# Optimization experiments

Hardware: AMD Instinct MI355X
Metric: run time of the kernel (lower is better)

Reference implementation:

```python
import jax, jax.numpy as jnp
import numpy as np

BATCH, SEQ, IN_DIM, HID, STATE, NLAYERS, OUT = 32, 2048, 32, 512, 64, 4, 2
EPS = 1e-5


def layer_norm(x, g, b):
    m = jnp.mean(x, axis=-1, keepdims=True)
    v = jnp.mean((x - m) ** 2, axis=-1, keepdims=True)
    return (x - m) / jnp.sqrt(v + EPS) * g + b


def s4_layer(x, A, C, D, g, b):
    # x: (B, L, H); A, C: (H, S); D: (H,)
    xn = layer_norm(x, g, b)
    u = jnp.swapaxes(xn, 0, 1)  # (L, B, H)

    def step(h, u_t):
        h = jnp.tanh(u_t @ A + h)          # (B, S)
        y = h @ C.T + u_t * D              # (B, H)
        return h, y

    h0 = jnp.zeros((x.shape[0], A.shape[1]), dtype=x.dtype)
    _, ys = jax.lax.scan(step, h0, u)
    return jnp.swapaxes(ys, 0, 1) + x      # residual


def setup_inputs() -> dict:
    key = jax.random.key(0)
    ks = jax.random.split(key, 16)
    s_in = 1.0 / np.sqrt(IN_DIM)
    s_h = 1.0 / np.sqrt(HID)
    s_h2 = 1.0 / np.sqrt(HID // 2)
    return {
        "x": jax.random.normal(ks[0], (BATCH, SEQ, IN_DIM), jnp.float32),
        "Win": jax.random.uniform(ks[1], (IN_DIM, HID), jnp.float32, -s_in, s_in),
        "bin_": jax.random.uniform(ks[2], (HID,), jnp.float32, -s_in, s_in),
        "A": jax.random.normal(ks[3], (NLAYERS, HID, STATE), jnp.float32) * 0.05,
        "C": jax.random.normal(ks[4], (NLAYERS, HID, STATE), jnp.float32) * 0.05,
        "Dvec": jax.random.normal(ks[5], (NLAYERS, HID), jnp.float32),
        "ln_g": jnp.ones((NLAYERS, HID), jnp.float32),
        "ln_b": jnp.zeros((NLAYERS, HID), jnp.float32),
        "norm_g": jnp.ones((HID,), jnp.float32),
        "norm_b": jnp.zeros((HID,), jnp.float32),
        "W1": jax.random.uniform(ks[6], (HID, HID // 2), jnp.float32, -s_h, s_h),
        "b1": jax.random.uniform(ks[7], (HID // 2,), jnp.float32, -s_h, s_h),
        "W2": jax.random.uniform(ks[8], (HID // 2, OUT), jnp.float32, -s_h2, s_h2),
        "b2": jax.random.uniform(ks[9], (OUT,), jnp.float32, -s_h2, s_h2),
    }


def reference(x, Win, bin_, A, C, Dvec, ln_g, ln_b, norm_g, norm_b, W1, b1, W2, b2):
    h = x @ Win + bin_                      # (B, L, H)
    for i in range(A.shape[0]):
        h = s4_layer(h, A[i], C[i], Dvec[i], ln_g[i], ln_b[i])
    h = layer_norm(h, norm_g, norm_b)
    h = h[:, -1, :]                         # last timestep
    h = jax.nn.gelu(h @ W1 + b1, approximate=False)  # torch nn.GELU uses erf
    return h @ W2 + b2
```

## Files before the change

### kernel.cpp

```cpp
#include <hip/hip_runtime.h>

#define BATCH   32
#define SEQ     2048
#define IN_DIM  32
#define HID     512
#define STATE   64
#define NLAYERS 4
#define NTOK    (BATCH*SEQ)
#define EPS     1e-5f
#define KTAN    2.8853900817779268f
#define NCHUNK  32
#define WARMUP  32

#define CF4(p) (*reinterpret_cast<const float4*>(p))

typedef __attribute__((ext_vector_type(8))) short short8v;
typedef __attribute__((ext_vector_type(4))) float f32x4;

__device__ __forceinline__ float fast_exp2(float x){ return __builtin_amdgcn_exp2f(x); }
__device__ __forceinline__ float fast_rcp(float x){ return __builtin_amdgcn_rcpf(x); }
__device__ __forceinline__ short f2bf(float f){
  unsigned u = __float_as_uint(f);
  unsigned r = (u + 0x7FFF + ((u>>16)&1)) >> 16;
  return (short)r;
}
__device__ __forceinline__ float bf2f(short s){
  return __uint_as_float(((unsigned)(unsigned short)s) << 16);
}

__global__ __launch_bounds__(256) void k_prep(
    const float* __restrict__ A, const float* __restrict__ g,
    const float* __restrict__ b, const float* __restrict__ Win,
    const float* __restrict__ bin, const float* __restrict__ C,
    short* __restrict__ ApT, float* __restrict__ GA, float* __restrict__ BA,
    short* __restrict__ WA1Th, short* __restrict__ WA1Tl,
    float* __restrict__ binA, short* __restrict__ Cb, short* __restrict__ WinT)
{
  __shared__ float red[4][64], red2[4][64];
  int tid = threadIdx.x;
  int s = tid & 63, part = tid >> 6;
  int blk = blockIdx.x;
  if (blk < NLAYERS){
    int l = blk;
    const float* Al = A + l*HID*STATE;
    const float* Cl = C + l*HID*STATE;
    const float* gl = g + l*HID;
    const float* bl = b + l*HID;
    float ga=0.f, ba=0.f;
    for (int j=part*128; j<(part+1)*128; ++j){
      float a  = Al[j*STATE+s];
      float ap = gl[j]*a;
      ApT[l*HID*STATE + s*HID + j] = f2bf(ap);
      Cb[l*HID*STATE + j*STATE + s] = f2bf(Cl[j*STATE+s]);
      ga += ap; ba = fmaf(bl[j], a, ba);
    }
    red[part][s]=ga; red2[part][s]=ba;
    __syncthreads();
    if (tid < 64){
      GA[l*STATE+s] = red[0][s]+red[1][s]+red[2][s]+red[3][s];
      BA[l*STATE+s] = red2[0][s]+red2[1][s]+red2[2][s]+red2[3][s];
    }
  } else if (blk < NLAYERS+32){
    int k = blk - NLAYERS;
    const float* w = Win + k*HID;
    float acc = 0.f;
    for (int j=part*128; j<(part+1)*128; ++j)
      acc = fmaf(w[j], g[j]*A[j*STATE+s], acc);
    red[part][s] = acc;
    __syncthreads();
    if (tid < 64){
      float v = red[0][s]+red[1][s]+red[2][s]+red[3][s];
      short hi = f2bf(v);
      WA1Th[s*IN_DIM + k] = hi;
      WA1Tl[s*IN_DIM + k] = f2bf(v - bf2f(hi));
    }
  } else if (blk == NLAYERS+32){
    float acc = 0.f;
    for (int j=part*128; j<(part+1)*128; ++j)
      acc = fmaf(bin[j], g[j]*A[j*STATE+s], acc);
    red[part][s] = acc;
    __syncthreads();
    if (tid < 64) binA[s] = red[0][s]+red[1][s]+red[2][s]+red[3][s];
  } else {
    for (int e = tid; e < HID*IN_DIM; e += 256){
      int cc = e >> 5, k = e & 31;
      WinT[cc*IN_DIM + k] = f2bf(Win[k*HID + cc]);
    }
  }
}

__global__ __launch_bounds__(256) void k_input(const float* __restrict__ x,
    const short* __restrict__ WinT, const float* __restrict__ bin,
    const short* __restrict__ WA1Th, const short* __restrict__ WA1Tl,
    const float* __restrict__ binA,
    const float* __restrict__ GA0, const float* __restrict__ BA0,
    short* __restrict__ h, float* __restrict__ U, float2* __restrict__ stats)
{
  __shared__ __align__(16) short xhi[64][72];
  __shared__ __align__(16) short xlo[64][72];
  int m0 = blockIdx.x * 64;
  int tid = threadIdx.x;
  int w = tid >> 6, lane = tid & 63;
  int c = lane & 15, q = lane >> 4;
  #pragma unroll
  for (int i=0;i<8;i++){
    int idx = tid + i*256;
    int row = idx >> 5, k = idx & 31;
    float v = x[(size_t)(m0+row)*IN_DIM + k];
    short hi = f2bf(v);
    xhi[row][k] = hi;
    xlo[row][k] = f2bf(v - bf2f(hi));
  }
  __syncthreads();
  short8v ah = *reinterpret_cast<const short8v*>(&xhi[w*16 + c][q*8]);
  short8v al = *reinterpret_cast<const short8v*>(&xlo[w*16 + c][q*8]);
  float sum[4]={0.f,0.f,0.f,0.f}, sq[4]={0.f,0.f,0.f,0.f};
  for (int jc=0; jc<HID; jc+=64){
    f32x4 acc[4];
    #pragma unroll
    for (int t=0;t<4;t++){
      short8v bv = *reinterpret_cast<const short8v*>(&WinT[(size_t)(jc + t*16 + c)*IN_DIM + q*8]);
      f32x4 a = {0.f,0.f,0.f,0.f};
      acc[t] = __builtin_amdgcn_mfma_f32_16x16x32_bf16(ah, bv, a, 0, 0, 0);
    }
    #pragma unroll
    for (int t=0;t<4;t++){
      int col = jc + t*16 + c;
      float bj = bin[col];
      #pragma unroll
      for (int r=0;r<4;r++){
        int m = m0 + w*16 + q*4 + r;
        float o = acc[t][r] + bj;
        h[(size_t)m*HID + col] = f2bf(o);
        sum[r] += o; sq[r] += o*o;
      }
    }
  }
  float mu[4], rs[4];
  #pragma unroll
  for (int r=0;r<4;r++){
    float s_ = sum[r], qq = sq[r];
    #pragma unroll
    for (int off=1; off<16; off<<=1){
      s_ += __shfl_xor(s_, off);
      qq += __shfl_xor(qq, off);
    }
    mu[r] = s_*(1.f/HID);
    float var = qq*(1.f/HID) - mu[r]*mu[r];
    rs[r] = rsqrtf(fmaxf(var,0.f)+EPS);
    if (c==0) stats[m0 + w*16 + q*4 + r] = make_float2(mu[r], rs[r]);
  }
  #pragma unroll
  for (int t=0;t<4;t++){
    short8v bh  = *reinterpret_cast<const short8v*>(&WA1Th[(size_t)(t*16 + c)*IN_DIM + q*8]);
    short8v blv = *reinterpret_cast<const short8v*>(&WA1Tl[(size_t)(t*16 + c)*IN_DIM + q*8]);
    f32x4 a = {0.f,0.f,0.f,0.f};
    a = __builtin_amdgcn_mfma_f32_16x16x32_bf16(ah, bh, a, 0, 0, 0);
    a = __builtin_amdgcn_mfma_f32_16x16x32_bf16(al, bh, a, 0, 0, 0);
    a = __builtin_amdgcn_mfma_f32_16x16x32_bf16(ah, blv, a, 0, 0, 0);
    int s = t*16 + c;
    float ga = GA0[s], ba = BA0[s], bA = binA[s];
    #pragma unroll
    for (int r=0;r<4;r++){
      int m = m0 + w*16 + q*4 + r;
      float u = a[r] + bA;
      U[(size_t)m*STATE + s] = fmaf(KTAN, rs[r]*(u - mu[r]*ga) + ba, KTAN);
    }
  }
}

__global__ __launch_bounds__(256) void k_ugemm(const short* __restrict__ hb,
    const float2* __restrict__ stats, const short* __restrict__ ApT,
    const float* __restrict__ GA, const float* __restrict__ BA,
    float* __restrict__ U)
{
  __shared__ __align__(16) short Hsh[64][72];
  __shared__ __align__(16) short Bsh[64][72];
  int m0 = blockIdx.x * 64;
  int tid = threadIdx.x;
  int w = tid >> 6, lane = tid & 63;
  int c = lane & 15, q = lane >> 4;
  float mu[4], rs[4];
  #pragma unroll
  for (int r=0;r<4;r++){
    float2 s2 = stats[m0 + w*16 + q*4 + r];
    mu[r]=s2.x; rs[r]=s2.y;
  }
  f32x4 acc[4] = {{0.f,0.f,0.f,0.f},{0.f,0.f,0.f,0.f},{0.f,0.f,0.f,0.f},{0.f,0.f,0.f,0.f}};
  for (int kc=0; kc<HID; kc+=64){
    #pragma unroll
    for (int p=0;p<2;p++){
      int idx = tid + p*256;
      int row = idx >> 3, kb = idx & 7;
      *reinterpret_cast<short8v*>(&Hsh[row][kb*8]) =
        *reinterpret_cast<const short8v*>(&hb[(size_t)(m0+row)*HID + kc + kb*8]);
      *reinterpret_cast<short8v*>(&Bsh[row][kb*8]) =
        *reinterpret_cast<const short8v*>(&ApT[(size_t)row*HID + kc + kb*8]);
    }
    __syncthreads();
    short8v a0 = *reinterpret_cast<const short8v*>(&Hsh[w*16 + c][q*8]);
    short8v a1 = *reinterpret_cast<const short8v*>(&Hsh[w*16 + c][32 + q*8]);
    #pragma unroll
    for (int t=0;t<4;t++){
      short8v b0 = *reinterpret_cast<const short8v*>(&Bsh[t*16 + c][q*8]);
      short8v b1 = *reinterpret_cast<const short8v*>(&Bsh[t*16 + c][32 + q*8]);
      acc[t] = __builtin_amdgcn_mfma_f32_16x16x32_bf16(a0, b0, acc[t], 0, 0, 0);
      acc[t] = __builtin_amdgcn_mfma_f32_16x16x32_bf16(a1, b1, acc[t], 0, 0, 0);
    }
    __syncthreads();
  }
  #pragma unroll
  for (int t=0;t<4;t++){
    int s = t*16 + c;
    float ga = GA[s], ba = BA[s];
    #pragma unroll
    for (int r=0;r<4;r++){
      int m = m0 + w*16 + q*4 + r;
      U[(size_t)m*STATE + s] = fmaf(KTAN, rs[r]*(acc[t][r] - mu[r]*ga) + ba, KTAN);
    }
  }
}

__global__ __launch_bounds__(64) void k_scan(const float* __restrict__ U,
                                             short* __restrict__ H)
{
  int b = blockIdx.x >> 5;
  int p = blockIdx.x & 31;
  int s = threadIdx.x;
  const float* Ub = U + (size_t)b*SEQ*STATE + s;
  short* Hb = H + (size_t)b*SEQ*STATE + s;
  float r = 0.5f;
  float cur[32], nxt[32];
  int t = (p == 0) ? 0 : (p*64 - WARMUP);
  int nsub = (p == 0) ? 2 : 3;
  #pragma unroll
  for (int i=0;i<32;i++) cur[i] = Ub[(t+i)*STATE];
  for (int cidx=0; cidx<nsub; ++cidx){
    bool has_next = (cidx+1 < nsub);
    if (has_next){
      #pragma unroll
      for (int i=0;i<32;i++) nxt[i] = Ub[(t+32+i)*STATE];
    }
    if ((p == 0) || (cidx > 0)){
      #pragma unroll
      for (int i=0;i<32;i++){
        float e = fast_exp2(fmaf(-2.f*KTAN, r, cur[i]));
        r = fast_rcp(1.f + e);
        Hb[(t+i)*STATE] = f2bf(fmaf(-2.f, r, 1.f));
      }
    } else {
      #pragma unroll
      for (int i=0;i<32;i++){
        float e = fast_exp2(fmaf(-2.f*KTAN, r, cur[i]));
        r = fast_rcp(1.f + e);
      }
    }
    if (has_next){
      #pragma unroll
      for (int i=0;i<32;i++) cur[i] = nxt[i];
    }
    t += 32;
  }
}

__global__ __launch_bounds__(256) void k_yep4(
    short* __restrict__ h, const short* __restrict__ Hg,
    const short* __restrict__ Cb, const float* __restrict__ Dl,
    const float* __restrict__ gl, const float* __restrict__ bl,
    const float2* __restrict__ stats_in, float2* __restrict__ stats_out)
{
  __shared__ __align__(16) short Hsh[64][72];
  __shared__ __align__(16) short Csh[64][72];
  __shared__ __align__(16) short Ysh[64][76];
  int m0 = blockIdx.x * 64;
  int tid = threadIdx.x;
  int w = tid >> 6, lane = tid & 63;
  int c = lane & 15, q = lane >> 4;
  int vrow = tid >> 3;
  int vcb  = tid & 7;
  #pragma unroll
  for (int p=0;p<2;p++){
    int idx = tid + p*256;
    int row = idx >> 3, kb = idx & 7;
    *reinterpret_cast<short8v*>(&Hsh[row][kb*8]) =
      *reinterpret_cast<const short8v*>(&Hg[(size_t)(m0+row)*STATE + kb*8]);
  }
  float2 sin0 = stats_in[m0 + vrow];
  float2 sin1 = stats_in[m0 + 32 + vrow];
  float sum0=0.f, sq0=0.f, sum1=0.f, sq1=0.f;
  __syncthreads();
  short8v a0 = *reinterpret_cast<const short8v*>(&Hsh[w*16 + c][q*8]);
  short8v a1 = *reinterpret_cast<const short8v*>(&Hsh[w*16 + c][32 + q*8]);
  for (int jc=0; jc<HID; jc+=64){
    #pragma unroll
    for (int p=0;p<2;p++){
      int idx = tid + p*256;
      int col = idx >> 3, kb = idx & 7;
      *reinterpret_cast<short8v*>(&Csh[col][kb*8]) =
        *reinterpret_cast<const short8v*>(&Cb[(size_t)(jc+col)*STATE + kb*8]);
    }
    __syncthreads();
    #pragma unroll
    for (int t=0;t<4;t++){
      short8v b0 = *reinterpret_cast<const short8v*>(&Csh[t*16 + c][q*8]);
      short8v b1 = *reinterpret_cast<const short8v*>(&Csh[t*16 + c][32 + q*8]);
      f32x4 a = {0.f,0.f,0.f,0.f};
      a = __builtin_amdgcn_mfma_f32_16x16x32_bf16(a0, b0, a, 0, 0, 0);
      a = __builtin_amdgcn_mfma_f32_16x16x32_bf16(a1, b1, a, 0, 0, 0);
      #pragma unroll
      for (int r=0;r<4;r++)
        Ysh[w*16 + q*4 + r][t*16 + c] = f2bf(a[r]);
    }
    __syncthreads();
    int col0 = jc + vcb*8;
    float4 gA = CF4(&gl[col0]), gB = CF4(&gl[col0+4]);
    float4 bA = CF4(&bl[col0]), bB = CF4(&bl[col0+4]);
    float4 dA = CF4(&Dl[col0]), dB = CF4(&Dl[col0+4]);
    float ga[8] = {gA.x,gA.y,gA.z,gA.w,gB.x,gB.y,gB.z,gB.w};
    float ba[8] = {bA.x,bA.y,bA.z,bA.w,bB.x,bB.y,bB.z,bB.w};
    float da[8] = {dA.x,dA.y,dA.z,dA.w,dB.x,dB.y,dB.z,dB.w};
    #pragma unroll
    for (int rep=0; rep<2; ++rep){
      int row = vrow + rep*32;
      int m = m0 + row;
      float mu_ = rep ? sin1.x : sin0.x;
      float rs_ = rep ? sin1.y : sin0.y;
      short8v hv = *reinterpret_cast<const short8v*>(&h[(size_t)m*HID + col0]);
      short8v yv = *reinterpret_cast<const short8v*>(&Ysh[row][vcb*8]);
      short8v ov;
      float lsum=0.f, lsq=0.f;
      #pragma unroll
      for (int i=0;i<8;i++){
        float hvf = bf2f(hv[i]);
        float o = hvf + bf2f(yv[i]) + fmaf((hvf-mu_)*rs_, ga[i], ba[i])*da[i];
        ov[i] = f2bf(o);
        lsum += o; lsq += o*o;
      }
      *reinterpret_cast<short8v*>(&h[(size_t)m*HID + col0]) = ov;
      if (rep) { sum1 += lsum; sq1 += lsq; } else { sum0 += lsum; sq0 += lsq; }
    }
  }
  #pragma unroll
  for (int off=1; off<8; off<<=1){
    sum0 += __shfl_xor(sum0, off);  sq0 += __shfl_xor(sq0, off);
    sum1 += __shfl_xor(sum1, off);  sq1 += __shfl_xor(sq1, off);
  }
  if (vcb == 0){
    float m0v = sum0*(1.f/HID);
    float v0 = sq0*(1.f/HID) - m0v*m0v;
    stats_out[m0 + vrow] = make_float2(m0v, rsqrtf(fmaxf(v0,0.f)+EPS));
    float m1v = sum1*(1.f/HID);
    float v1 = sq1*(1.f/HID) - m1v*m1v;
    stats_out[m0 + 32 + vrow] = make_float2(m1v, rsqrtf(fmaxf(v1,0.f)+EPS));
  }
}

__global__ __launch_bounds__(256) void k_head(const short* __restrict__ h,
   const float2* __restrict__ stats, const float* __restrict__ ng, const float* __restrict__ nb,
   const float* __restrict__ W1, const float* __restrict__ b1,
   const float* __restrict__ W2, const float* __restrict__ b2,
   float* __restrict__ out)
{
  int bb = blockIdx.x;
  int m = bb*SEQ + (SEQ-1);
  int tid = threadIdx.x;
  __shared__ float xs[HID];
  __shared__ float red[8];
  float2 st = stats[m];
  #pragma unroll
  for (int i=0;i<2;i++){
    int j = tid + i*256;
    float v = bf2f(h[(size_t)m*HID + j]);
    xs[j] = fmaf((v - st.x)*st.y, ng[j], nb[j]);
  }
  __syncthreads();
  float acc = b1[tid];
  #pragma unroll 8
  for (int j=0;j<HID;j++) acc = fmaf(xs[j], W1[j*(HID/2) + tid], acc);
  float ge = 0.5f*acc*(1.f + erff(acc*0.70710678118654752f));
  float p0 = ge*W2[tid*2+0];
  float p1 = ge*W2[tid*2+1];
  #pragma unroll
  for (int off=32; off; off>>=1){ p0 += __shfl_down(p0, off); p1 += __shfl_down(p1, off); }
  int wid = tid>>6;
  if ((tid&63)==0){ red[wid*2]=p0; red[wid*2+1]=p1; }
  __syncthreads();
  if (tid==0){
    float o0=b2[0], o1=b2[1];
    #pragma unroll
    for (int w=0;w<4;w++){ o0+=red[w*2]; o1+=red[w*2+1]; }
    out[bb*2+0]=o0; out[bb*2+1]=o1;
  }
}

extern "C" void kernel_launch(void* const* d_in, const int* in_sizes, int n_in,
                              void* d_out, int out_size, void* d_ws, size_t ws_size,
                              hipStream_t stream)
{
  (void)in_sizes; (void)n_in; (void)out_size; (void)ws_size;
  const float* x   = (const float*)d_in[0];
  const float* Win = (const float*)d_in[1];
  const float* bin = (const float*)d_in[2];
  const float* A   = (const float*)d_in[3];
  const float* C   = (const float*)d_in[4];
  const float* Dv  = (const float*)d_in[5];
  const float* lng = (const float*)d_in[6];
  const float* lnb = (const float*)d_in[7];
  const float* ng  = (const float*)d_in[8];
  const float* nb  = (const float*)d_in[9];
  const float* W1  = (const float*)d_in[10];
  const float* b1  = (const float*)d_in[11];
  const float* W2  = (const float*)d_in[12];
  const float* b2  = (const float*)d_in[13];
  float* out = (float*)d_out;
  char* ws = (char*)d_ws;
  short*  hb   = (short*)(ws + 0);
  float*  Ubuf = (float*)(ws + (size_t)67108864);
  short*  Hbuf = (short*)(ws + (size_t)83886080);
  float2* st0  = (float2*)(ws + (size_t)92274688);
  float2* st1  = (float2*)(ws + (size_t)92798976);
  short*  ApT  = (short*)(ws + (size_t)93323264);
  float*  GAb  = (float*)(ws + (size_t)93585408);
  float*  BAb  = (float*)(ws + (size_t)93586432);
  float*  binAb= (float*)(ws + (size_t)93587456);
  short*  Cb   = (short*)(ws + (size_t)93587712);
  short*  WinT = (short*)(ws + (size_t)93849856);
  short*  WA1Th= (short*)(ws + (size_t)93882624);
  short*  WA1Tl= (short*)(ws + (size_t)93886720);

  hipLaunchKernelGGL(k_prep,  dim3(38), dim3(256), 0, stream,
      A, lng, lnb, Win, bin, C, ApT, GAb, BAb, WA1Th, WA1Tl, binAb, Cb, WinT);
  hipLaunchKernelGGL(k_input, dim3(NTOK/64), dim3(256), 0, stream,
      x, WinT, bin, WA1Th, WA1Tl, binAb, GAb, BAb, hb, Ubuf, st0);
  float2* scur = st0; float2* snxt = st1;
  for (int l=0; l<NLAYERS; ++l){
    if (l > 0){
      hipLaunchKernelGGL(k_ugemm, dim3(NTOK/64), dim3(256), 0, stream,
          hb, scur, ApT + l*HID*STATE, GAb + l*STATE, BAb + l*STATE, Ubuf);
    }
    hipLaunchKernelGGL(k_scan, dim3(BATCH*NCHUNK), dim3(64), 0, stream, Ubuf, Hbuf);
    hipLaunchKernelGGL(k_yep4, dim3(NTOK/64), dim3(256), 0, stream,
        hb, Hbuf, Cb + l*HID*STATE, Dv + l*HID, lng + l*HID, lnb + l*HID, scur, snxt);
    float2* t = scur; scur = snxt; snxt = t;
  }
  hipLaunchKernelGGL(k_head, dim3(BATCH), dim3(256), 0, stream,
      hb, scur, ng, nb, W1, b1, W2, b2, out);
}
```

Measured before the change: 253.4 us.

## Fuse next-layer U GEMM into y-epilogue kernel and drop separate ugemm pass

Removes the standalone k_ugemm kernel by computing the next layer's state projection inside the y-epilogue kernel. The freshly written hidden row tile is kept in LDS (a full 32x512 bf16 tile), so h does not have to be re-read from global memory for the next layer's input. To fit this, the epilogue tile shrinks to 32 rows and each wave now owns a column block instead of a row block. The input kernel is also restructured to stage bf16 outputs through LDS for vectorized stores and row statistics. This saves one kernel launch and one full pass over h per layer, at the cost of more LDS per block (lower occupancy), extra barriers, and half-sized tiles.

```diff
diff --git a/kernel.cpp b/kernel.cpp
--- a/kernel.cpp
+++ b/kernel.cpp
@@ -98,10 +98,13 @@
 {
   __shared__ __align__(16) short xhi[64][72];
   __shared__ __align__(16) short xlo[64][72];
+  __shared__ __align__(16) short Ysh[64][76];
+  __shared__ float2 statS[64];
   int m0 = blockIdx.x * 64;
   int tid = threadIdx.x;
   int w = tid >> 6, lane = tid & 63;
   int c = lane & 15, q = lane >> 4;
+  int vrow = tid >> 3, vcb = tid & 7;
   #pragma unroll
   for (int i=0;i<8;i++){
     int idx = tid + i*256;
@@ -114,41 +117,57 @@
   __syncthreads();
   short8v ah = *reinterpret_cast<const short8v*>(&xhi[w*16 + c][q*8]);
   short8v al = *reinterpret_cast<const short8v*>(&xlo[w*16 + c][q*8]);
-  float sum[4]={0.f,0.f,0.f,0.f}, sq[4]={0.f,0.f,0.f,0.f};
+  float sum0=0.f, sq0=0.f, sum1=0.f, sq1=0.f;
   for (int jc=0; jc<HID; jc+=64){
-    f32x4 acc[4];
     #pragma unroll
     for (int t=0;t<4;t++){
       short8v bv = *reinterpret_cast<const short8v*>(&WinT[(size_t)(jc + t*16 + c)*IN_DIM + q*8]);
       f32x4 a = {0.f,0.f,0.f,0.f};
-      acc[t] = __builtin_amdgcn_mfma_f32_16x16x32_bf16(ah, bv, a, 0, 0, 0);
-    }
-    #pragma unroll
-    for (int t=0;t<4;t++){
+      a = __builtin_amdgcn_mfma_f32_16x16x32_bf16(ah, bv, a, 0, 0, 0);
       int col = jc + t*16 + c;
       float bj = bin[col];
       #pragma unroll
-      for (int r=0;r<4;r++){
-        int m = m0 + w*16 + q*4 + r;
-        float o = acc[t][r] + bj;
-        h[(size_t)m*HID + col] = f2bf(o);
-        sum[r] += o; sq[r] += o*o;
-      }
-    }
-  }
+      for (int r=0;r<4;r++)
+        Ysh[w*16 + q*4 + r][t*16 + c] = f2bf(a[r] + bj);
+    }
+    __syncthreads();
+    #pragma unroll
+    for (int rep=0; rep<2; ++rep){
+      int row = vrow + rep*32;
+      int m = m0 + row;
+      short8v yv = *reinterpret_cast<const short8v*>(&Ysh[row][vcb*8]);
+      *reinterpret_cast<short8v*>(&h[(size_t)m*HID + jc + vcb*8]) = yv;
+      float lsum=0.f, lsq=0.f;
+      #pragma unroll
+      for (int i=0;i<8;i++){
+        float o = bf2f(yv[i]);
+        lsum += o; lsq += o*o;
+      }
+      if (rep) { sum1 += lsum; sq1 += lsq; } else { sum0 += lsum; sq0 += lsq; }
+    }
+    __syncthreads();
+  }
+  #pragma unroll
+  for (int off=1; off<8; off<<=1){
+    sum0 += __shfl_xor(sum0, off);  sq0 += __shfl_xor(sq0, off);
+    sum1 += __shfl_xor(sum1, off);  sq1 += __shfl_xor(sq1, off);
+  }
+  if (vcb == 0){
+    float m0v = sum0*(1.f/HID);
+    float v0 = sq0*(1.f/HID) - m0v*m0v;
+    float2 s0 = make_float2(m0v, rsqrtf(fmaxf(v0,0.f)+EPS));
+    stats[m0 + vrow] = s0;  statS[vrow] = s0;
+    float m1v = sum1*(1.f/HID);
+    float v1 = sq1*(1.f/HID) - m1v*m1v;
+    float2 s1 = make_float2(m1v, rsqrtf(fmaxf(v1,0.f)+EPS));
+    stats[m0 + 32 + vrow] = s1;  statS[32 + vrow] = s1;
+  }
+  __syncthreads();
   float mu[4], rs[4];
   #pragma unroll
   for (int r=0;r<4;r++){
-    float s_ = sum[r], qq = sq[r];
-    #pragma unroll
-    for (int off=1; off<16; off<<=1){
-      s_ += __shfl_xor(s_, off);
-      qq += __shfl_xor(qq, off);
-    }
-    mu[r] = s_*(1.f/HID);
-    float var = qq*(1.f/HID) - mu[r]*mu[r];
-    rs[r] = rsqrtf(fmaxf(var,0.f)+EPS);
-    if (c==0) stats[m0 + w*16 + q*4 + r] = make_float2(mu[r], rs[r]);
+    float2 s2 = statS[w*16 + q*4 + r];
+    mu[r]=s2.x; rs[r]=s2.y;
   }
   #pragma unroll
   for (int t=0;t<4;t++){
@@ -169,58 +188,6 @@
   }
 }
 
-__global__ __launch_bounds__(256) void k_ugemm(const short* __restrict__ hb,
-    const float2* __restrict__ stats, const short* __restrict__ ApT,
-    const float* __restrict__ GA, const float* __restrict__ BA,
-    float* __restrict__ U)
-{
-  __shared__ __align__(16) short Hsh[64][72];
-  __shared__ __align__(16) short Bsh[64][72];
-  int m0 = blockIdx.x * 64;
-  int tid = threadIdx.x;
-  int w = tid >> 6, lane = tid & 63;
-  int c = lane & 15, q = lane >> 4;
-  float mu[4], rs[4];
-  #pragma unroll
-  for (int r=0;r<4;r++){
-    float2 s2 = stats[m0 + w*16 + q*4 + r];
-    mu[r]=s2.x; rs[r]=s2.y;
-  }
-  f32x4 acc[4] = {{0.f,0.f,0.f,0.f},{0.f,0.f,0.f,0.f},{0.f,0.f,0.f,0.f},{0.f,0.f,0.f,0.f}};
-  for (int kc=0; kc<HID; kc+=64){
-    #pragma unroll
-    for (int p=0;p<2;p++){
-      int idx = tid + p*256;
-      int row = idx >> 3, kb = idx & 7;
-      *reinterpret_cast<short8v*>(&Hsh[row][kb*8]) =
-        *reinterpret_cast<const short8v*>(&hb[(size_t)(m0+row)*HID + kc + kb*8]);
-      *reinterpret_cast<short8v*>(&Bsh[row][kb*8]) =
-        *reinterpret_cast<const short8v*>(&ApT[(size_t)row*HID + kc + kb*8]);
-    }
-    __syncthreads();
-    short8v a0 = *reinterpret_cast<const short8v*>(&Hsh[w*16 + c][q*8]);
-    short8v a1 = *reinterpret_cast<const short8v*>(&Hsh[w*16 + c][32 + q*8]);
-    #pragma unroll
-    for (int t=0;t<4;t++){
-      short8v b0 = *reinterpret_cast<const short8v*>(&Bsh[t*16 + c][q*8]);
-      short8v b1 = *reinterpret_cast<const short8v*>(&Bsh[t*16 + c][32 + q*8]);
-      acc[t] = __builtin_amdgcn_mfma_f32_16x16x32_bf16(a0, b0, acc[t], 0, 0, 0);
-      acc[t] = __builtin_amdgcn_mfma_f32_16x16x32_bf16(a1, b1, acc[t], 0, 0, 0);
-    }
-    __syncthreads();
-  }
-  #pragma unroll
-  for (int t=0;t<4;t++){
-    int s = t*16 + c;
-    float ga = GA[s], ba = BA[s];
-    #pragma unroll
-    for (int r=0;r<4;r++){
-      int m = m0 + w*16 + q*4 + r;
-      U[(size_t)m*STATE + s] = fmaf(KTAN, rs[r]*(acc[t][r] - mu[r]*ga) + ba, KTAN);
-    }
-  }
-}
-
 __global__ __launch_bounds__(64) void k_scan(const float* __restrict__ U,
                                              short* __restrict__ H)
 {
@@ -263,34 +230,36 @@
   }
 }
 
-__global__ __launch_bounds__(256) void k_yep4(
+__global__ __launch_bounds__(256) void k_yep5(
     short* __restrict__ h, const short* __restrict__ Hg,
     const short* __restrict__ Cb, const float* __restrict__ Dl,
     const float* __restrict__ gl, const float* __restrict__ bl,
-    const float2* __restrict__ stats_in, float2* __restrict__ stats_out)
-{
-  __shared__ __align__(16) short Hsh[64][72];
+    const float2* __restrict__ stats_in, float2* __restrict__ stats_out,
+    const short* __restrict__ ApTn, const float* __restrict__ GAn,
+    const float* __restrict__ BAn, float* __restrict__ U, int has_next)
+{
+  __shared__ __align__(16) short Hsh[32][72];
   __shared__ __align__(16) short Csh[64][72];
-  __shared__ __align__(16) short Ysh[64][76];
-  int m0 = blockIdx.x * 64;
+  __shared__ __align__(16) short Ysh[32][76];
+  __shared__ __align__(16) short hful[32][528];
+  __shared__ float2 statS[32];
+  int m0 = blockIdx.x * 32;
   int tid = threadIdx.x;
   int w = tid >> 6, lane = tid & 63;
   int c = lane & 15, q = lane >> 4;
-  int vrow = tid >> 3;
-  int vcb  = tid & 7;
-  #pragma unroll
-  for (int p=0;p<2;p++){
-    int idx = tid + p*256;
-    int row = idx >> 3, kb = idx & 7;
+  int vrow = tid >> 3, vcb = tid & 7;
+  {
+    int row = tid >> 3, kb = tid & 7;
     *reinterpret_cast<short8v*>(&Hsh[row][kb*8]) =
       *reinterpret_cast<const short8v*>(&Hg[(size_t)(m0+row)*STATE + kb*8]);
   }
-  float2 sin0 = stats_in[m0 + vrow];
-  float2 sin1 = stats_in[m0 + 32 + vrow];
-  float sum0=0.f, sq0=0.f, sum1=0.f, sq1=0.f;
-  __syncthreads();
-  short8v a0 = *reinterpret_cast<const short8v*>(&Hsh[w*16 + c][q*8]);
-  short8v a1 = *reinterpret_cast<const short8v*>(&Hsh[w*16 + c][32 + q*8]);
+  float2 sin = stats_in[m0 + vrow];
+  float sum=0.f, sq=0.f;
+  __syncthreads();
+  short8v a00 = *reinterpret_cast<const short8v*>(&Hsh[c][q*8]);
+  short8v a01 = *reinterpret_cast<const short8v*>(&Hsh[c][32 + q*8]);
+  short8v a10 = *reinterpret_cast<const short8v*>(&Hsh[16 + c][q*8]);
+  short8v a11 = *reinterpret_cast<const short8v*>(&Hsh[16 + c][32 + q*8]);
   for (int jc=0; jc<HID; jc+=64){
     #pragma unroll
     for (int p=0;p<2;p++){
@@ -300,16 +269,20 @@
         *reinterpret_cast<const short8v*>(&Cb[(size_t)(jc+col)*STATE + kb*8]);
     }
     __syncthreads();
-    #pragma unroll
-    for (int t=0;t<4;t++){
-      short8v b0 = *reinterpret_cast<const short8v*>(&Csh[t*16 + c][q*8]);
-      short8v b1 = *reinterpret_cast<const short8v*>(&Csh[t*16 + c][32 + q*8]);
-      f32x4 a = {0.f,0.f,0.f,0.f};
-      a = __builtin_amdgcn_mfma_f32_16x16x32_bf16(a0, b0, a, 0, 0, 0);
-      a = __builtin_amdgcn_mfma_f32_16x16x32_bf16(a1, b1, a, 0, 0, 0);
-      #pragma unroll
-      for (int r=0;r<4;r++)
-        Ysh[w*16 + q*4 + r][t*16 + c] = f2bf(a[r]);
+    {
+      short8v b0 = *reinterpret_cast<const short8v*>(&Csh[w*16 + c][q*8]);
+      short8v b1 = *reinterpret_cast<const short8v*>(&Csh[w*16 + c][32 + q*8]);
+      f32x4 acc0 = {0.f,0.f,0.f,0.f};
+      acc0 = __builtin_amdgcn_mfma_f32_16x16x32_bf16(a00, b0, acc0, 0, 0, 0);
+      acc0 = __builtin_amdgcn_mfma_f32_16x16x32_bf16(a01, b1, acc0, 0, 0, 0);
+      f32x4 acc1 = {0.f,0.f,0.f,0.f};
+      acc1 = __builtin_amdgcn_mfma_f32_16x16x32_bf16(a10, b0, acc1, 0, 0, 0);
+      acc1 = __builtin_amdgcn_mfma_f32_16x16x32_bf16(a11, b1, acc1, 0, 0, 0);
+      #pragma unroll
+      for (int r=0;r<4;r++){
+        Ysh[q*4 + r][w*16 + c]      = f2bf(acc0[r]);
+        Ysh[16 + q*4 + r][w*16 + c] = f2bf(acc1[r]);
+      }
     }
     __syncthreads();
     int col0 = jc + vcb*8;
@@ -319,39 +292,60 @@
     float ga[8] = {gA.x,gA.y,gA.z,gA.w,gB.x,gB.y,gB.z,gB.w};
     float ba[8] = {bA.x,bA.y,bA.z,bA.w,bB.x,bB.y,bB.z,bB.w};
     float da[8] = {dA.x,dA.y,dA.z,dA.w,dB.x,dB.y,dB.z,dB.w};
-    #pragma unroll
-    for (int rep=0; rep<2; ++rep){
-      int row = vrow + rep*32;
-      int m = m0 + row;
-      float mu_ = rep ? sin1.x : sin0.x;
-      float rs_ = rep ? sin1.y : sin0.y;
+    {
+      int m = m0 + vrow;
       short8v hv = *reinterpret_cast<const short8v*>(&h[(size_t)m*HID + col0]);
-      short8v yv = *reinterpret_cast<const short8v*>(&Ysh[row][vcb*8]);
+      short8v yv = *reinterpret_cast<const short8v*>(&Ysh[vrow][vcb*8]);
       short8v ov;
-      float lsum=0.f, lsq=0.f;
       #pragma unroll
       for (int i=0;i<8;i++){
         float hvf = bf2f(hv[i]);
-        float o = hvf + bf2f(yv[i]) + fmaf((hvf-mu_)*rs_, ga[i], ba[i])*da[i];
+        float o = hvf + bf2f(yv[i]) + fmaf((hvf-sin.x)*sin.y, ga[i], ba[i])*da[i];
         ov[i] = f2bf(o);
-        lsum += o; lsq += o*o;
+        sum += o; sq += o*o;
       }
       *reinterpret_cast<short8v*>(&h[(size_t)m*HID + col0]) = ov;
-      if (rep) { sum1 += lsum; sq1 += lsq; } else { sum0 += lsum; sq0 += lsq; }
-    }
+      *reinterpret_cast<short8v*>(&hful[vrow][col0]) = ov;
+    }
+    __syncthreads();
   }
   #pragma unroll
   for (int off=1; off<8; off<<=1){
-    sum0 += __shfl_xor(sum0, off);  sq0 += __shfl_xor(sq0, off);
-    sum1 += __shfl_xor(sum1, off);  sq1 += __shfl_xor(sq1, off);
+    sum += __shfl_xor(sum, off);  sq += __shfl_xor(sq, off);
   }
   if (vcb == 0){
-    float m0v = sum0*(1.f/HID);
-    float v0 = sq0*(1.f/HID) - m0v*m0v;
-    stats_out[m0 + vrow] = make_float2(m0v, rsqrtf(fmaxf(v0,0.f)+EPS));
-    float m1v = sum1*(1.f/HID);
-    float v1 = sq1*(1.f/HID) - m1v*m1v;
-    stats_out[m0 + 32 + vrow] = make_float2(m1v, rsqrtf(fmaxf(v1,0.f)+EPS));
+    float mv = sum*(1.f/HID);
+    float vv = sq*(1.f/HID) - mv*mv;
+    float2 s2 = make_float2(mv, rsqrtf(fmaxf(vv,0.f)+EPS));
+    stats_out[m0 + vrow] = s2;
+    statS[vrow] = s2;
+  }
+  __syncthreads();
+  if (has_next){
+    f32x4 u0 = {0.f,0.f,0.f,0.f}, u1 = {0.f,0.f,0.f,0.f};
+    int sI = w*16 + c;
+    const short* Bp = ApTn + (size_t)sI*HID;
+    for (int kc=0; kc<HID; kc+=32){
+      short8v bfr = *reinterpret_cast<const short8v*>(Bp + kc + q*8);
+      short8v ag0 = *reinterpret_cast<const short8v*>(&hful[c][kc + q*8]);
+      short8v ag1 = *reinterpret_cast<const short8v*>(&hful[16 + c][kc + q*8]);
+      u0 = __builtin_amdgcn_mfma_f32_16x16x32_bf16(ag0, bfr, u0, 0, 0, 0);
+      u1 = __builtin_amdgcn_mfma_f32_16x16x32_bf16(ag1, bfr, u1, 0, 0, 0);
+    }
+    float ga = GAn[sI], ba = BAn[sI];
+    #pragma unroll
+    for (int r=0;r<4;r++){
+      {
+        int row = q*4 + r;
+        float2 st = statS[row];
+        U[(size_t)(m0+row)*STATE + sI] = fmaf(KTAN, st.y*(u0[r] - st.x*ga) + ba, KTAN);
+      }
+      {
+        int row = 16 + q*4 + r;
+        float2 st = statS[row];
+        U[(size_t)(m0+row)*STATE + sI] = fmaf(KTAN, st.y*(u1[r] - st.x*ga) + ba, KTAN);
+      }
+    }
   }
 }
 
@@ -434,13 +428,13 @@
       x, WinT, bin, WA1Th, WA1Tl, binAb, GAb, BAb, hb, Ubuf, st0);
   float2* scur = st0; float2* snxt = st1;
   for (int l=0; l<NLAYERS; ++l){
-    if (l > 0){
-      hipLaunchKernelGGL(k_ugemm, dim3(NTOK/64), dim3(256), 0, stream,
-          hb, scur, ApT + l*HID*STATE, GAb + l*STATE, BAb + l*STATE, Ubuf);
-    }
+    int has_next = (l < NLAYERS-1) ? 1 : 0;
+    int ln = has_next ? (l+1) : 0;
     hipLaunchKernelGGL(k_scan, dim3(BATCH*NCHUNK), dim3(64), 0, stream, Ubuf, Hbuf);
-    hipLaunchKernelGGL(k_yep4, dim3(NTOK/64), dim3(256), 0, stream,
-        hb, Hbuf, Cb + l*HID*STATE, Dv + l*HID, lng + l*HID, lnb + l*HID, scur, snxt);
+    hipLaunchKernelGGL(k_yep5, dim3(NTOK/32), dim3(256), 0, stream,
+        hb, Hbuf, Cb + l*HID*STATE, Dv + l*HID, lng + l*HID, lnb + l*HID,
+        scur, snxt, ApT + ln*HID*STATE, GAb + ln*STATE, BAb + ln*STATE,
+        Ubuf, has_next);
     float2* t = scur; scur = snxt; snxt = t;
   }
   hipLaunchKernelGGL(k_head, dim3(BATCH), dim3(256), 0, stream,
```

Measured after the change: 291.4 us. 15.0% more time.

## Fuse next-layer U projection into epilogue kernel and stage input-layer stores through LDS

Applied to the files above, without the earlier changes.

Removes the separate k_ugemm launch. The epilogue kernel now computes the next layer's U = LN(h)@A projection right after writing h, reading its freshly written rows of h from global/L2 and stats from LDS. It also restructures k_input to stage outputs through shared memory, giving vectorized h stores and row-stat reductions. This saves three kernel launches and some re-reading of h and stats. In exchange the fused kernel uses more registers and LDS, and the input kernel adds extra barriers.

```diff
diff --git a/kernel.cpp b/kernel.cpp
--- a/kernel.cpp
+++ b/kernel.cpp
@@ -98,10 +98,13 @@
 {
   __shared__ __align__(16) short xhi[64][72];
   __shared__ __align__(16) short xlo[64][72];
+  __shared__ __align__(16) short Ysh[64][76];
+  __shared__ float2 statS[64];
   int m0 = blockIdx.x * 64;
   int tid = threadIdx.x;
   int w = tid >> 6, lane = tid & 63;
   int c = lane & 15, q = lane >> 4;
+  int vrow = tid >> 3, vcb = tid & 7;
   #pragma unroll
   for (int i=0;i<8;i++){
     int idx = tid + i*256;
@@ -114,41 +117,57 @@
   __syncthreads();
   short8v ah = *reinterpret_cast<const short8v*>(&xhi[w*16 + c][q*8]);
   short8v al = *reinterpret_cast<const short8v*>(&xlo[w*16 + c][q*8]);
-  float sum[4]={0.f,0.f,0.f,0.f}, sq[4]={0.f,0.f,0.f,0.f};
+  float sum0=0.f, sq0=0.f, sum1=0.f, sq1=0.f;
   for (int jc=0; jc<HID; jc+=64){
-    f32x4 acc[4];
     #pragma unroll
     for (int t=0;t<4;t++){
       short8v bv = *reinterpret_cast<const short8v*>(&WinT[(size_t)(jc + t*16 + c)*IN_DIM + q*8]);
       f32x4 a = {0.f,0.f,0.f,0.f};
-      acc[t] = __builtin_amdgcn_mfma_f32_16x16x32_bf16(ah, bv, a, 0, 0, 0);
-    }
-    #pragma unroll
-    for (int t=0;t<4;t++){
+      a = __builtin_amdgcn_mfma_f32_16x16x32_bf16(ah, bv, a, 0, 0, 0);
       int col = jc + t*16 + c;
       float bj = bin[col];
       #pragma unroll
-      for (int r=0;r<4;r++){
-        int m = m0 + w*16 + q*4 + r;
-        float o = acc[t][r] + bj;
-        h[(size_t)m*HID + col] = f2bf(o);
-        sum[r] += o; sq[r] += o*o;
+      for (int r=0;r<4;r++)
+        Ysh[w*16 + q*4 + r][t*16 + c] = f2bf(a[r] + bj);
+    }
+    __syncthreads();
+    #pragma unroll
+    for (int rep=0; rep<2; ++rep){
+      int row = vrow + rep*32;
+      int m = m0 + row;
+      short8v yv = *reinterpret_cast<const short8v*>(&Ysh[row][vcb*8]);
+      *reinterpret_cast<short8v*>(&h[(size_t)m*HID + jc + vcb*8]) = yv;
+      float lsum=0.f, lsq=0.f;
+      #pragma unroll
+      for (int i=0;i<8;i++){
+        float o = bf2f(yv[i]);
+        lsum += o; lsq += o*o;
       }
-    }
-  }
+      if (rep) { sum1 += lsum; sq1 += lsq; } else { sum0 += lsum; sq0 += lsq; }
+    }
+    __syncthreads();
+  }
+  #pragma unroll
+  for (int off=1; off<8; off<<=1){
+    sum0 += __shfl_xor(sum0, off);  sq0 += __shfl_xor(sq0, off);
+    sum1 += __shfl_xor(sum1, off);  sq1 += __shfl_xor(sq1, off);
+  }
+  if (vcb == 0){
+    float m0v = sum0*(1.f/HID);
+    float v0 = sq0*(1.f/HID) - m0v*m0v;
+    float2 s0 = make_float2(m0v, rsqrtf(fmaxf(v0,0.f)+EPS));
+    stats[m0 + vrow] = s0;  statS[vrow] = s0;
+    float m1v = sum1*(1.f/HID);
+    float v1 = sq1*(1.f/HID) - m1v*m1v;
+    float2 s1 = make_float2(m1v, rsqrtf(fmaxf(v1,0.f)+EPS));
+    stats[m0 + 32 + vrow] = s1;  statS[32 + vrow] = s1;
+  }
+  __syncthreads();
   float mu[4], rs[4];
   #pragma unroll
   for (int r=0;r<4;r++){
-    float s_ = sum[r], qq = sq[r];
-    #pragma unroll
-    for (int off=1; off<16; off<<=1){
-      s_ += __shfl_xor(s_, off);
-      qq += __shfl_xor(qq, off);
-    }
-    mu[r] = s_*(1.f/HID);
-    float var = qq*(1.f/HID) - mu[r]*mu[r];
-    rs[r] = rsqrtf(fmaxf(var,0.f)+EPS);
-    if (c==0) stats[m0 + w*16 + q*4 + r] = make_float2(mu[r], rs[r]);
+    float2 s2 = statS[w*16 + q*4 + r];
+    mu[r]=s2.x; rs[r]=s2.y;
   }
   #pragma unroll
   for (int t=0;t<4;t++){
@@ -169,58 +188,6 @@
   }
 }
 
-__global__ __launch_bounds__(256) void k_ugemm(const short* __restrict__ hb,
-    const float2* __restrict__ stats, const short* __restrict__ ApT,
-    const float* __restrict__ GA, const float* __restrict__ BA,
-    float* __restrict__ U)
-{
-  __shared__ __align__(16) short Hsh[64][72];
-  __shared__ __align__(16) short Bsh[64][72];
-  int m0 = blockIdx.x * 64;
-  int tid = threadIdx.x;
-  int w = tid >> 6, lane = tid & 63;
-  int c = lane & 15, q = lane >> 4;
-  float mu[4], rs[4];
-  #pragma unroll
-  for (int r=0;r<4;r++){
-    float2 s2 = stats[m0 + w*16 + q*4 + r];
-    mu[r]=s2.x; rs[r]=s2.y;
-  }
-  f32x4 acc[4] = {{0.f,0.f,0.f,0.f},{0.f,0.f,0.f,0.f},{0.f,0.f,0.f,0.f},{0.f,0.f,0.f,0.f}};
-  for (int kc=0; kc<HID; kc+=64){
-    #pragma unroll
-    for (int p=0;p<2;p++){
-      int idx = tid + p*256;
-      int row = idx >> 3, kb = idx & 7;
-      *reinterpret_cast<short8v*>(&Hsh[row][kb*8]) =
-        *reinterpret_cast<const short8v*>(&hb[(size_t)(m0+row)*HID + kc + kb*8]);
-      *reinterpret_cast<short8v*>(&Bsh[row][kb*8]) =
-        *reinterpret_cast<const short8v*>(&ApT[(size_t)row*HID + kc + kb*8]);
-    }
-    __syncthreads();
-    short8v a0 = *reinterpret_cast<const short8v*>(&Hsh[w*16 + c][q*8]);
-    short8v a1 = *reinterpret_cast<const short8v*>(&Hsh[w*16 + c][32 + q*8]);
-    #pragma unroll
-    for (int t=0;t<4;t++){
-      short8v b0 = *reinterpret_cast<const short8v*>(&Bsh[t*16 + c][q*8]);
-      short8v b1 = *reinterpret_cast<const short8v*>(&Bsh[t*16 + c][32 + q*8]);
-      acc[t] = __builtin_amdgcn_mfma_f32_16x16x32_bf16(a0, b0, acc[t], 0, 0, 0);
-      acc[t] = __builtin_amdgcn_mfma_f32_16x16x32_bf16(a1, b1, acc[t], 0, 0, 0);
-    }
-    __syncthreads();
-  }
-  #pragma unroll
-  for (int t=0;t<4;t++){
-    int s = t*16 + c;
-    float ga = GA[s], ba = BA[s];
-    #pragma unroll
-    for (int r=0;r<4;r++){
-      int m = m0 + w*16 + q*4 + r;
-      U[(size_t)m*STATE + s] = fmaf(KTAN, rs[r]*(acc[t][r] - mu[r]*ga) + ba, KTAN);
-    }
-  }
-}
-
 __global__ __launch_bounds__(64) void k_scan(const float* __restrict__ U,
                                              short* __restrict__ H)
 {
@@ -263,15 +230,18 @@
   }
 }
 
-__global__ __launch_bounds__(256) void k_yep4(
+__global__ __launch_bounds__(256) void k_yep6(
     short* __restrict__ h, const short* __restrict__ Hg,
     const short* __restrict__ Cb, const float* __restrict__ Dl,
     const float* __restrict__ gl, const float* __restrict__ bl,
-    const float2* __restrict__ stats_in, float2* __restrict__ stats_out)
+    const float2* __restrict__ stats_in, float2* __restrict__ stats_out,
+    const short* __restrict__ ApTn, const float* __restrict__ GAn,
+    const float* __restrict__ BAn, float* __restrict__ U, int has_next)
 {
   __shared__ __align__(16) short Hsh[64][72];
   __shared__ __align__(16) short Csh[64][72];
   __shared__ __align__(16) short Ysh[64][76];
+  __shared__ float2 statS[64];
   int m0 = blockIdx.x * 64;
   int tid = threadIdx.x;
   int w = tid >> 6, lane = tid & 63;
@@ -348,10 +318,42 @@
   if (vcb == 0){
     float m0v = sum0*(1.f/HID);
     float v0 = sq0*(1.f/HID) - m0v*m0v;
-    stats_out[m0 + vrow] = make_float2(m0v, rsqrtf(fmaxf(v0,0.f)+EPS));
+    float2 s0 = make_float2(m0v, rsqrtf(fmaxf(v0,0.f)+EPS));
+    stats_out[m0 + vrow] = s0;  statS[vrow] = s0;
     float m1v = sum1*(1.f/HID);
     float v1 = sq1*(1.f/HID) - m1v*m1v;
-    stats_out[m0 + 32 + vrow] = make_float2(m1v, rsqrtf(fmaxf(v1,0.f)+EPS));
+    float2 s1 = make_float2(m1v, rsqrtf(fmaxf(v1,0.f)+EPS));
+    stats_out[m0 + 32 + vrow] = s1;  statS[32 + vrow] = s1;
+  }
+  if (!has_next) return;
+  __syncthreads();
+  f32x4 uacc[4] = {{0.f,0.f,0.f,0.f},{0.f,0.f,0.f,0.f},
+                   {0.f,0.f,0.f,0.f},{0.f,0.f,0.f,0.f}};
+  for (int kc=0; kc<HID; kc+=32){
+    short8v a = *reinterpret_cast<const short8v*>(
+        &h[(size_t)(m0 + w*16 + c)*HID + kc + q*8]);
+    #pragma unroll
+    for (int t=0;t<4;t++){
+      short8v bb = *reinterpret_cast<const short8v*>(
+          &ApTn[(size_t)(t*16 + c)*HID + kc + q*8]);
+      uacc[t] = __builtin_amdgcn_mfma_f32_16x16x32_bf16(a, bb, uacc[t], 0, 0, 0);
+    }
+  }
+  float mu[4], rs[4];
+  #pragma unroll
+  for (int r=0;r<4;r++){
+    float2 s2 = statS[w*16 + q*4 + r];
+    mu[r]=s2.x; rs[r]=s2.y;
+  }
+  #pragma unroll
+  for (int t=0;t<4;t++){
+    int sI = t*16 + c;
+    float ga = GAn[sI], ba = BAn[sI];
+    #pragma unroll
+    for (int r=0;r<4;r++){
+      int m = m0 + w*16 + q*4 + r;
+      U[(size_t)m*STATE + sI] = fmaf(KTAN, rs[r]*(uacc[t][r] - mu[r]*ga) + ba, KTAN);
+    }
   }
 }
 
@@ -434,13 +436,13 @@
       x, WinT, bin, WA1Th, WA1Tl, binAb, GAb, BAb, hb, Ubuf, st0);
   float2* scur = st0; float2* snxt = st1;
   for (int l=0; l<NLAYERS; ++l){
-    if (l > 0){
-      hipLaunchKernelGGL(k_ugemm, dim3(NTOK/64), dim3(256), 0, stream,
-          hb, scur, ApT + l*HID*STATE, GAb + l*STATE, BAb + l*STATE, Ubuf);
-    }
+    int has_next = (l < NLAYERS-1) ? 1 : 0;
+    int ln = has_next ? (l+1) : 0;
     hipLaunchKernelGGL(k_scan, dim3(BATCH*NCHUNK), dim3(64), 0, stream, Ubuf, Hbuf);
-    hipLaunchKernelGGL(k_yep4, dim3(NTOK/64), dim3(256), 0, stream,
-        hb, Hbuf, Cb + l*HID*STATE, Dv + l*HID, lng + l*HID, lnb + l*HID, scur, snxt);
+    hipLaunchKernelGGL(k_yep6, dim3(NTOK/64), dim3(256), 0, stream,
+        hb, Hbuf, Cb + l*HID*STATE, Dv + l*HID, lng + l*HID, lnb + l*HID,
+        scur, snxt, ApT + ln*HID*STATE, GAb + ln*STATE, BAb + ln*STATE,
+        Ubuf, has_next);
     float2* t = scur; scur = snxt; snxt = t;
   }
   hipLaunchKernelGGL(k_head, dim3(BATCH), dim3(256), 0, stream,
```

Measured after the change: 307.5 us. 1.21x slower.
